# Performance work log

Measured on AMD Instinct MI355X. Metric: run time of the kernel, lower is better.

## Reference

```python
import jax, jax.numpy as jnp
import numpy as np

OBS, ACT, NTRAIN, BATCH = 8, 4, 128, 8
DIN = OBS + ACT


def setup_inputs() -> dict:
    key = jax.random.key(0)
    ks = jax.random.split(key, 11)
    f32 = jnp.float32
    m_x = jax.random.normal(ks[0], (BATCH, OBS), dtype=f32)
    A = 0.1 * jax.random.normal(ks[1], (BATCH, OBS, OBS), dtype=f32)
    s_x = A @ jnp.swapaxes(A, -1, -2) + 0.01 * jnp.eye(OBS, dtype=f32)  # SPD obs covariance
    m_u = jax.random.normal(ks[2], (BATCH, ACT), dtype=f32)
    Au = 0.1 * jax.random.normal(ks[3], (BATCH, ACT, ACT), dtype=f32)
    s_u = Au @ jnp.swapaxes(Au, -1, -2) + 0.01 * jnp.eye(ACT, dtype=f32)
    c_xu = 0.05 * jax.random.normal(ks[4], (BATCH, OBS, ACT), dtype=f32)
    X_train = jax.random.normal(ks[5], (NTRAIN, DIN), dtype=f32)
    lengthscales = jax.random.uniform(ks[6], (OBS, DIN), dtype=f32, minval=0.5, maxval=2.0)
    variances = jax.random.uniform(ks[7], (OBS, 1), dtype=f32, minval=0.5, maxval=1.5)
    noises = jax.random.uniform(ks[8], (OBS,), dtype=f32, minval=0.01, maxval=0.1)
    R = jax.random.normal(ks[9], (OBS, NTRAIN, NTRAIN), dtype=f32) / np.float32(np.sqrt(NTRAIN))
    inv_K = R @ jnp.swapaxes(R, -1, -2) + 0.1 * jnp.eye(NTRAIN, dtype=f32)  # SPD like a true K^-1
    beta = 0.1 * jax.random.normal(ks[10], (OBS, NTRAIN), dtype=f32)
    return dict(m_x=m_x, s_x=s_x, m_u=m_u, s_u=s_u, c_xu=c_xu, X_train=X_train,
                lengthscales=lengthscales, variances=variances, noises=noises,
                inv_K=inv_K, beta=beta)


def _forward(m_x, s_x, m_u, s_u, c_xu, X_train, lengthscales, variances, noises, inv_K, beta):
    obs_dim, input_dim = lengthscales.shape
    n = X_train.shape[0]
    eyeD = jnp.eye(input_dim, dtype=m_x.dtype)
    # joint input distribution over [x, u]
    joint_mean = jnp.concatenate([m_x, m_u], axis=-1)                      # [B, D]
    s_ = s_x @ c_xu                                                        # [B, obs, act] (as in source)
    upper = jnp.concatenate([s_x, s_], axis=-1)                            # [B, obs, D]
    lower = jnp.concatenate([jnp.swapaxes(s_, -1, -2), s_u], axis=-1)      # [B, act, D]
    joint_var = jnp.concatenate([upper, lower], axis=-2)                   # [B, D, D]
    # --- predictive mean (moment matching) ---
    inp = X_train[None, :, :] - joint_mean[:, None, :]                     # [B, N, D]
    inv_ls = 1.0 / lengthscales                                            # [E, D]
    inv_N = inp[:, None, :, :] * inv_ls[None, :, None, :]                  # [B, E, N, D]
    B_mat = inv_ls[None, :, :, None] * joint_var[:, None, :, :] * inv_ls[None, :, None, :] + eyeD
    t = jnp.swapaxes(jnp.linalg.solve(B_mat, jnp.swapaxes(inv_N, -1, -2)), -1, -2)  # [B, E, N, D]
    scaled_exp = jnp.exp(-0.5 * jnp.sum(inv_N * t, axis=-1))               # [B, E, N]
    lb = scaled_exp * beta[None, :, :]                                     # [B, E, N]
    det_B = jnp.linalg.det(B_mat)                                          # [B, E]
    var_v = variances[:, 0]                                                # [E]
    c = var_v[None, :] / jnp.sqrt(det_B)                                   # [B, E]
    pred_mean = jnp.sum(lb, axis=-1) * c                                   # [B, E]
    # --- input-output cross covariance ---
    t_inv_L = t * inv_ls[None, :, None, :]                                 # [B, E, N, D]
    cross_cov = jnp.swapaxes(jnp.einsum('bend,ben->bed', t_inv_L, lb) * c[..., None], -1, -2)  # [B, D, E]
    # --- predictive covariance: vectorized over all (a, b) output pairs ---
    X_i = X_train[:, None, :]
    X_j = X_train[None, :, :]
    diff = X_i - X_j                                                       # [N, N, D]
    l2 = lengthscales ** 2
    inv_l2 = 1.0 / l2

    def pair(l2_a, inv_a, var_a, beta_a, l2_b, inv_b, var_b, beta_b):
        inv_sum = inv_a + inv_b                                            # [D]
        Lam = 1.0 / inv_sum
        z_bar = Lam * (X_i * inv_a + X_j * inv_b)                          # [N, N, D]
        z = z_bar[None, :, :, :] - joint_mean[:, None, None, :]            # [B, N, N, D]
        z_flat = z.reshape(z.shape[0], n * n, input_dim)
        R_ab = joint_var * inv_sum[None, None, :] + eyeD                   # joint_var @ diag(inv_sum) + I
        exp1 = -0.5 * jnp.sum(diff * diff * (1.0 / (l2_a + l2_b)), axis=-1)  # [N, N]
        M_ab = joint_var + jnp.diag(Lam)[None, :, :]                       # [B, D, D]
        solved = jnp.swapaxes(jnp.linalg.solve(M_ab, jnp.swapaxes(z_flat, -1, -2)), -1, -2)
        exp2 = (-0.5 * jnp.sum(z_flat * solved, axis=-1)).reshape(z.shape[0], n, n)
        c_ab = var_a * var_b / jnp.sqrt(jnp.linalg.det(R_ab))              # [B]
        Q = c_ab[:, None, None] * jnp.exp(exp1[None, :, :] + exp2)         # [B, N, N]
        main = jnp.einsum('i,bij,j->b', beta_a, Q, beta_b)                 # [B]
        return main, Q

    pair_b = jax.vmap(pair, in_axes=(None, None, None, None, 0, 0, 0, 0))
    pair_ab = jax.vmap(pair_b, in_axes=(0, 0, 0, 0, None, None, None, None))
    main, Q = pair_ab(l2, inv_l2, var_v, beta, l2, inv_l2, var_v, beta)    # [E, E, B], [E, E, B, N, N]
    pred_cov = jnp.moveaxis(main, -1, 0)                                   # [B, E, E]
    idx = jnp.arange(obs_dim)
    Q_diag = Q[idx, idx]                                                   # [E, B, N, N]
    trace_val = jnp.einsum('eij,ebji->eb', inv_K, Q_diag)                  # [E, B]
    diag_corr = var_v[:, None] - trace_val + noises[:, None]               # [E, B]
    pred_cov = pred_cov + diag_corr.T[:, :, None] * jnp.eye(obs_dim, dtype=m_x.dtype)
    pred_cov = pred_cov - pred_mean[:, :, None] * pred_mean[:, None, :]
    pred_cov = 0.5 * (pred_cov + jnp.swapaxes(pred_cov, -1, -2))
    # --- propagate state moments ---
    cov_xf = upper @ cross_cov                                             # [B, obs, obs]
    m_out = m_x + pred_mean
    s_out = s_x + pred_cov + cov_xf + jnp.swapaxes(cov_xf, -1, -2)
    s_out = 0.5 * (s_out + jnp.swapaxes(s_out, -1, -2)) + 1e-8 * jnp.eye(obs_dim, dtype=m_x.dtype)
    return m_out, s_out


def reference(m_x, s_x, m_u, s_u, c_xu, X_train, lengthscales, variances, noises, inv_K, beta):
    return _forward(m_x, s_x, m_u, s_u, c_xu, X_train, lengthscales, variances, noises, inv_K, beta)
```

## Files before the change

### kernel.cpp

```cpp
#include <hip/hip_runtime.h>
#include <math.h>

#define OBS 8
#define ACT 4
#define DIN 12
#define NTRAIN 128
#define BATCH 8
#define NPAIR 36
#define NPT (BATCH*NPAIR)
#define NGT (BATCH*OBS)
#define NTASK (NPT+NGT)

#define WS_PM  0
#define WS_CC  64
#define WS_MN  832
#define WS_TR  1344

__global__ void __launch_bounds__(256) k_fused(
    const float* __restrict__ m_x, const float* __restrict__ s_x,
    const float* __restrict__ m_u, const float* __restrict__ s_u,
    const float* __restrict__ c_xu, const float* __restrict__ X,
    const float* __restrict__ ls, const float* __restrict__ vars,
    const float* __restrict__ beta, const float* __restrict__ invK,
    float* __restrict__ ws)
{
    int blk = blockIdx.x, tid = threadIdx.x;
    bool isPair = blk < NPT;
    int b, a = 0, c = 0, e = 0;
    if (isPair) {
        b = blk / NPAIR;
        int rem = blk % NPAIR;
        while (rem >= OBS - a) { rem -= OBS - a; a++; }
        c = a + rem;
    } else {
        int q = blk - NPT; b = q / OBS; e = q % OBS;
    }

    __shared__ float jvs[144];
    __shared__ float Wl[144];
    __shared__ float mu[DIN];
    __shared__ float sc_wsum[DIN], sc_iA[DIN], sc_qc[DIN], sc_lam[DIN], sc_isum[DIN];
    __shared__ float s_cab;
    __shared__ __align__(16) float h[NTRAIN][12];
    __shared__ float basei[NTRAIN], wav[NTRAIN];
    __shared__ float red[4][13];

    if (tid < 144) {
        int r = tid / 12, cl = tid % 12;
        float v;
        if (r < OBS && cl < OBS) {
            v = s_x[(b*OBS+r)*OBS + cl];
        } else if (r < OBS) {
            v = 0.f;
            #pragma unroll
            for (int k = 0; k < OBS; k++)
                v += s_x[(b*OBS+r)*OBS+k] * c_xu[(b*OBS+k)*ACT + (cl-OBS)];
        } else if (cl < OBS) {
            v = 0.f;
            #pragma unroll
            for (int k = 0; k < OBS; k++)
                v += s_x[(b*OBS+cl)*OBS+k] * c_xu[(b*OBS+k)*ACT + (r-OBS)];
        } else {
            v = s_u[(b*ACT+r-OBS)*ACT + (cl-OBS)];
        }
        jvs[tid] = v;
    } else if (tid >= 160 && tid < 172) {
        int d = tid - 160;
        mu[d] = (d < OBS) ? m_x[b*OBS+d] : m_u[b*ACT+d-OBS];
    } else if (tid >= 192 && tid < 204) {
        int d = tid - 192;
        if (isPair) {
            float la = ls[a*DIN+d]; la *= la;
            float lc = ls[c*DIN+d]; lc *= lc;
            float ia = 1.f/la, ic = 1.f/lc;
            float is = ia + ic;
            float L  = 1.f/is;
            sc_wsum[d] = 1.f/(la+lc);
            sc_iA[d] = L*ia;
            sc_qc[d] = L*ic;
            sc_lam[d] = L;
            sc_isum[d] = is;
        } else {
            sc_iA[d] = 1.f / ls[e*DIN+d];
        }
    }
    __syncthreads();

    if (tid < DIN) {
        int r = tid;
        float row[12];
        if (isPair) {
            #pragma unroll
            for (int j = 0; j < 12; j++) row[j] = jvs[r*12+j];
            row[r] += sc_lam[r];
        } else {
            float ir = sc_iA[r];
            #pragma unroll
            for (int j = 0; j < 12; j++) row[j] = ir * sc_iA[j] * jvs[r*12+j];
            row[r] += 1.f;
        }
        float det = 1.f;
        #pragma unroll
        for (int k = 0; k < 12; k++) {
            float p = __shfl(row[k], k);
            float ip = 1.f / p;
            det *= p;
            float prow[12];
            #pragma unroll
            for (int j = 0; j < 12; j++) prow[j] = __shfl(row[j], k) * ip;
            if (r == k) {
                #pragma unroll
                for (int j = 0; j < 12; j++) row[j] = prow[j];
                row[k] = ip;
            } else {
                float f = row[k];
                #pragma unroll
                for (int j = 0; j < 12; j++) if (j != k) row[j] -= f * prow[j];
                row[k] = -f * ip;
            }
        }
        #pragma unroll
        for (int j = 0; j < 12; j++) Wl[r*12+j] = row[j];
        if (r == 0) {
            if (isPair) {
                float s = det;
                #pragma unroll
                for (int d = 0; d < 12; d++) s *= sc_isum[d];
                s_cab = vars[a]*vars[c] / sqrtf(s);
            } else {
                s_cab = vars[e] / sqrtf(det);
            }
        }
    }
    __syncthreads();

    if (isPair) {
        bool diag = (a == c);
        if (tid < NTRAIN) {
            int i = tid;
            const float4* xr = (const float4*)(X + i*DIN);
            float4 x0 = xr[0], x1 = xr[1], x2 = xr[2];
            float x[12] = {x0.x,x0.y,x0.z,x0.w, x1.x,x1.y,x1.z,x1.w, x2.x,x2.y,x2.z,x2.w};
            float r[12]; float e1 = 0.f;
            #pragma unroll
            for (int d = 0; d < 12; d++) {
                r[d] = sc_iA[d]*x[d] - mu[d];
                e1 += sc_wsum[d]*x[d]*x[d];
            }
            float alpha = 0.f;
            #pragma unroll
            for (int d = 0; d < 12; d++) {
                float u = 0.f;
                #pragma unroll
                for (int cl = 0; cl < 12; cl++) u += Wl[d*12+cl]*r[cl];
                alpha += r[d]*u;
                h[i][d] = sc_wsum[d]*x[d] - u*sc_qc[d];
            }
            basei[i] = -0.5f*(e1 + alpha);
            wav[i] = beta[a*NTRAIN+i];
        }
        int j = tid & 127;
        float xj[12], basej, wc;
        {
            const float4* xr = (const float4*)(X + j*DIN);
            float4 x0 = xr[0], x1 = xr[1], x2 = xr[2];
            xj[0]=x0.x; xj[1]=x0.y; xj[2]=x0.z; xj[3]=x0.w;
            xj[4]=x1.x; xj[5]=x1.y; xj[6]=x1.z; xj[7]=x1.w;
            xj[8]=x2.x; xj[9]=x2.y; xj[10]=x2.z; xj[11]=x2.w;
            float q[12]; float e1 = 0.f;
            #pragma unroll
            for (int d = 0; d < 12; d++) {
                q[d] = sc_qc[d]*xj[d];
                e1 += sc_wsum[d]*xj[d]*xj[d];
            }
            float bq = 0.f;
            #pragma unroll
            for (int d = 0; d < 12; d++) {
                float u = 0.f;
                #pragma unroll
                for (int cl = 0; cl < 12; cl++) u += Wl[d*12+cl]*q[cl];
                bq += q[d]*u;
            }
            basej = -0.5f*(e1 + bq);
            wc = beta[c*NTRAIN+j];
        }
        __syncthreads();
        float accm = 0.f, acct = 0.f;
        const float* Ka = invK + a*NTRAIN*NTRAIN;
        int ip = tid >> 7;
        #pragma unroll 8
        for (int k = 0; k < 64; k++) {
            int i = ip + 2*k;
            const float4* hp = (const float4*)(&h[i][0]);
            float4 h0 = hp[0], h1 = hp[1], h2 = hp[2];
            float sA = fmaf(h0.x,xj[0], fmaf(h0.y,xj[1], fmaf(h0.z,xj[2], h0.w*xj[3])));
            float sB = fmaf(h1.x,xj[4], fmaf(h1.y,xj[5], fmaf(h1.z,xj[6], h1.w*xj[7])));
            float sC = fmaf(h2.x,xj[8], fmaf(h2.y,xj[9], fmaf(h2.z,xj[10], h2.w*xj[11])));
            float ev = __expf(sA + sB + sC + basei[i] + basej);
            accm = fmaf(wav[i], ev, accm);
            if (diag) acct = fmaf(Ka[i*NTRAIN+j], ev, acct);
        }
        accm *= wc;
        #pragma unroll
        for (int off = 32; off >= 1; off >>= 1) {
            accm += __shfl_xor(accm, off, 64);
            acct += __shfl_xor(acct, off, 64);
        }
        int wv = tid >> 6, lane = tid & 63;
        if (lane == 0) { red[wv][0] = accm; red[wv][1] = acct; }
        __syncthreads();
        if (tid == 0) {
            float cab = s_cab;
            float m = (red[0][0]+red[1][0]+red[2][0]+red[3][0]) * cab;
            ws[WS_MN + b*64 + a*8 + c] = m;
            ws[WS_MN + b*64 + c*8 + a] = m;
            if (diag)
                ws[WS_TR + b*8 + a] = (red[0][1]+red[1][1]+red[2][1]+red[3][1]) * cab;
        }
    } else {
        float vals[13];
        #pragma unroll
        for (int v = 0; v < 13; v++) vals[v] = 0.f;
        if (tid < NTRAIN) {
            int n = tid;
            const float4* xr = (const float4*)(X + n*DIN);
            float4 x0 = xr[0], x1 = xr[1], x2 = xr[2];
            float x[12] = {x0.x,x0.y,x0.z,x0.w, x1.x,x1.y,x1.z,x1.w, x2.x,x2.y,x2.z,x2.w};
            float iN[12];
            #pragma unroll
            for (int d = 0; d < 12; d++) iN[d] = (x[d]-mu[d]) * sc_iA[d];
            float qq = 0.f; float tv[12];
            #pragma unroll
            for (int d = 0; d < 12; d++) {
                float u = 0.f;
                #pragma unroll
                for (int cl = 0; cl < 12; cl++) u += Wl[d*12+cl]*iN[cl];
                tv[d] = u; qq += iN[d]*u;
            }
            float lb = __expf(-0.5f*qq) * beta[e*NTRAIN+n];
            vals[0] = lb;
            #pragma unroll
            for (int d = 0; d < 12; d++) vals[1+d] = tv[d]*sc_iA[d]*lb;
        }
        #pragma unroll
        for (int v = 0; v < 13; v++)
            #pragma unroll
            for (int off = 32; off >= 1; off >>= 1) vals[v] += __shfl_xor(vals[v], off, 64);
        int wv = tid >> 6, lane = tid & 63;
        if (lane == 0) {
            #pragma unroll
            for (int v = 0; v < 13; v++) red[wv][v] = vals[v];
        }
        __syncthreads();
        if (tid == 0) {
            float cn = s_cab;
            ws[WS_PM + b*OBS + e] = cn*(red[0][0]+red[1][0]+red[2][0]+red[3][0]);
            for (int d = 0; d < 12; d++)
                ws[WS_CC + (b*DIN+d)*OBS + e] =
                    cn*(red[0][1+d]+red[1][1+d]+red[2][1+d]+red[3][1+d]);
        }
    }
}

__global__ void k_final(const float* __restrict__ m_x, const float* __restrict__ s_x,
                        const float* __restrict__ c_xu, const float* __restrict__ vars,
                        const float* __restrict__ noises, const float* __restrict__ ws,
                        float* __restrict__ out) {
    int b = blockIdx.x, t = threadIdx.x;
    __shared__ float pm[OBS];
    __shared__ float sxs[64];
    const float* cc = ws + WS_CC + b*DIN*OBS;
    const float* mn = ws + WS_MN + b*64;
    const float* tr = ws + WS_TR + b*OBS;
    sxs[t] = s_x[b*64 + t];
    if (t < OBS) {
        float p = ws[WS_PM + b*OBS + t];
        pm[t] = p;
        out[b*OBS + t] = m_x[b*OBS + t] + p;
    }
    __syncthreads();
    int r = t >> 3, cl = t & 7;
    float P = mn[r*8 + cl];
    if (r == cl) P += vars[r] - tr[r] + noises[r];
    P -= pm[r]*pm[cl];
    float cxf = 0.f, cxfT = 0.f;
    #pragma unroll
    for (int d = 0; d < 8; d++) {
        cxf  += sxs[r*8+d]  * cc[d*8+cl];
        cxfT += sxs[cl*8+d] * cc[d*8+r];
    }
    #pragma unroll
    for (int d = 0; d < 4; d++) {
        float jr = 0.f, jc = 0.f;
        #pragma unroll
        for (int k = 0; k < 8; k++) {
            float cx = c_xu[(b*OBS+k)*ACT + d];
            jr += sxs[r*8+k]  * cx;
            jc += sxs[cl*8+k] * cx;
        }
        cxf  += jr * cc[(8+d)*8 + cl];
        cxfT += jc * cc[(8+d)*8 + r];
    }
    float S = sxs[r*8+cl] + P + cxf + cxfT;
    if (r == cl) S += 1e-8f;
    out[64 + b*64 + t] = S;
}

extern "C" void kernel_launch(void* const* d_in, const int* in_sizes, int n_in,
                              void* d_out, int out_size, void* d_ws, size_t ws_size,
                              hipStream_t stream) {
    const float* m_x    = (const float*)d_in[0];
    const float* s_x    = (const float*)d_in[1];
    const float* m_u    = (const float*)d_in[2];
    const float* s_u    = (const float*)d_in[3];
    const float* c_xu   = (const float*)d_in[4];
    const float* X      = (const float*)d_in[5];
    const float* ls     = (const float*)d_in[6];
    const float* vars   = (const float*)d_in[7];
    const float* noises = (const float*)d_in[8];
    const float* invK   = (const float*)d_in[9];
    const float* beta   = (const float*)d_in[10];
    float* out = (float*)d_out;
    float* ws  = (float*)d_ws;

    k_fused<<<NTASK, 256, 0, stream>>>(m_x, s_x, m_u, s_u, c_xu, X, ls, vars, beta, invK, ws);
    k_final<<<BATCH, 64, 0, stream>>>(m_x, s_x, c_xu, vars, noises, ws, out);
}
```

Measured before the change: 103.5 us.

## Fuse final kernel via last-block atomic counter and widen blocks to 512 threads

Merges the separate finalisation kernel into the main kernel: each block publishes its results with agent-scope atomic stores, increments a global counter, and the last block to finish computes the output covariance and mean. Blocks also double from 256 to 512 threads, halving the per-thread loop over training points in the pair tasks. This removes one kernel launch and its dependency gap, but adds a memset launch, fences and atomics. The non-pair branch now reduces only two wave partials, which assumes the work still fits in the first 128 threads.

```diff
diff --git a/kernel.cpp b/kernel.cpp
--- a/kernel.cpp
+++ b/kernel.cpp
@@ -10,19 +10,29 @@
 #define NPT (BATCH*NPAIR)
 #define NGT (BATCH*OBS)
 #define NTASK (NPT+NGT)
+#define THREADS 512
 
 #define WS_PM  0
 #define WS_CC  64
 #define WS_MN  832
 #define WS_TR  1344
-
-__global__ void __launch_bounds__(256) k_fused(
+#define WS_CNT 1408
+
+__device__ __forceinline__ float agload(const float* p) {
+    return __hip_atomic_load(p, __ATOMIC_RELAXED, __HIP_MEMORY_SCOPE_AGENT);
+}
+__device__ __forceinline__ void agstore(float* p, float v) {
+    __hip_atomic_store(p, v, __ATOMIC_RELAXED, __HIP_MEMORY_SCOPE_AGENT);
+}
+
+__global__ void __launch_bounds__(THREADS) k_all(
     const float* __restrict__ m_x, const float* __restrict__ s_x,
     const float* __restrict__ m_u, const float* __restrict__ s_u,
     const float* __restrict__ c_xu, const float* __restrict__ X,
     const float* __restrict__ ls, const float* __restrict__ vars,
-    const float* __restrict__ beta, const float* __restrict__ invK,
-    float* __restrict__ ws)
+    const float* __restrict__ noises, const float* __restrict__ beta,
+    const float* __restrict__ invK, float* __restrict__ ws,
+    float* __restrict__ out)
 {
     int blk = blockIdx.x, tid = threadIdx.x;
     bool isPair = blk < NPT;
@@ -43,7 +53,8 @@
     __shared__ float s_cab;
     __shared__ __align__(16) float h[NTRAIN][12];
     __shared__ float basei[NTRAIN], wav[NTRAIN];
-    __shared__ float red[4][13];
+    __shared__ float red[8][13];
+    __shared__ unsigned s_last;
 
     if (tid < 144) {
         int r = tid / 12, cl = tid % 12;
@@ -189,8 +200,8 @@
         const float* Ka = invK + a*NTRAIN*NTRAIN;
         int ip = tid >> 7;
         #pragma unroll 8
-        for (int k = 0; k < 64; k++) {
-            int i = ip + 2*k;
+        for (int k = 0; k < 32; k++) {
+            int i = ip + 4*k;
             const float4* hp = (const float4*)(&h[i][0]);
             float4 h0 = hp[0], h1 = hp[1], h2 = hp[2];
             float sA = fmaf(h0.x,xj[0], fmaf(h0.y,xj[1], fmaf(h0.z,xj[2], h0.w*xj[3])));
@@ -210,12 +221,13 @@
         if (lane == 0) { red[wv][0] = accm; red[wv][1] = acct; }
         __syncthreads();
         if (tid == 0) {
-            float cab = s_cab;
-            float m = (red[0][0]+red[1][0]+red[2][0]+red[3][0]) * cab;
-            ws[WS_MN + b*64 + a*8 + c] = m;
-            ws[WS_MN + b*64 + c*8 + a] = m;
-            if (diag)
-                ws[WS_TR + b*8 + a] = (red[0][1]+red[1][1]+red[2][1]+red[3][1]) * cab;
+            float m = 0.f, t = 0.f;
+            #pragma unroll
+            for (int w = 0; w < 8; w++) { m += red[w][0]; t += red[w][1]; }
+            m *= s_cab; t *= s_cab;
+            agstore(ws + WS_MN + b*64 + a*8 + c, m);
+            agstore(ws + WS_MN + b*64 + c*8 + a, m);
+            if (diag) agstore(ws + WS_TR + b*8 + a, t);
         }
     } else {
         float vals[13];
@@ -254,56 +266,62 @@
         __syncthreads();
         if (tid == 0) {
             float cn = s_cab;
-            ws[WS_PM + b*OBS + e] = cn*(red[0][0]+red[1][0]+red[2][0]+red[3][0]);
+            agstore(ws + WS_PM + b*OBS + e, cn*(red[0][0]+red[1][0]));
             for (int d = 0; d < 12; d++)
-                ws[WS_CC + (b*DIN+d)*OBS + e] =
-                    cn*(red[0][1+d]+red[1][1+d]+red[2][1+d]+red[3][1+d]);
-        }
-    }
-}
-
-__global__ void k_final(const float* __restrict__ m_x, const float* __restrict__ s_x,
-                        const float* __restrict__ c_xu, const float* __restrict__ vars,
-                        const float* __restrict__ noises, const float* __restrict__ ws,
-                        float* __restrict__ out) {
-    int b = blockIdx.x, t = threadIdx.x;
-    __shared__ float pm[OBS];
-    __shared__ float sxs[64];
-    const float* cc = ws + WS_CC + b*DIN*OBS;
-    const float* mn = ws + WS_MN + b*64;
-    const float* tr = ws + WS_TR + b*OBS;
-    sxs[t] = s_x[b*64 + t];
-    if (t < OBS) {
-        float p = ws[WS_PM + b*OBS + t];
-        pm[t] = p;
-        out[b*OBS + t] = m_x[b*OBS + t] + p;
+                agstore(ws + WS_CC + (b*DIN+d)*OBS + e, cn*(red[0][1+d]+red[1][1+d]));
+        }
+    }
+
+    __threadfence();
+    if (tid == 0) {
+        unsigned* cnt = (unsigned*)(ws + WS_CNT);
+        unsigned old = __hip_atomic_fetch_add(cnt, 1u, __ATOMIC_ACQ_REL,
+                                              __HIP_MEMORY_SCOPE_AGENT);
+        s_last = (old == NTASK - 1) ? 1u : 0u;
     }
     __syncthreads();
-    int r = t >> 3, cl = t & 7;
-    float P = mn[r*8 + cl];
-    if (r == cl) P += vars[r] - tr[r] + noises[r];
-    P -= pm[r]*pm[cl];
-    float cxf = 0.f, cxfT = 0.f;
-    #pragma unroll
-    for (int d = 0; d < 8; d++) {
-        cxf  += sxs[r*8+d]  * cc[d*8+cl];
-        cxfT += sxs[cl*8+d] * cc[d*8+r];
-    }
-    #pragma unroll
-    for (int d = 0; d < 4; d++) {
-        float jr = 0.f, jc = 0.f;
-        #pragma unroll
-        for (int k = 0; k < 8; k++) {
-            float cx = c_xu[(b*OBS+k)*ACT + d];
-            jr += sxs[r*8+k]  * cx;
-            jc += sxs[cl*8+k] * cx;
-        }
-        cxf  += jr * cc[(8+d)*8 + cl];
-        cxfT += jc * cc[(8+d)*8 + r];
-    }
-    float S = sxs[r*8+cl] + P + cxf + cxfT;
-    if (r == cl) S += 1e-8f;
-    out[64 + b*64 + t] = S;
+    if (s_last) {
+        __threadfence();
+        int bb = tid >> 6, t = tid & 63;
+        int r = t >> 3, cl = t & 7;
+        const float* pm = ws + WS_PM + bb*OBS;
+        const float* cc = ws + WS_CC + bb*DIN*OBS;
+        const float* mn = ws + WS_MN + bb*64;
+        const float* tr = ws + WS_TR + bb*OBS;
+        if (t < OBS)
+            out[bb*OBS + t] = m_x[bb*OBS + t] + agload(pm + t);
+        float pmr = agload(pm + r), pmc = agload(pm + cl);
+        float P = agload(mn + r*8 + cl);
+        if (r == cl) P += vars[r] - agload(tr + r) + noises[r];
+        P -= pmr * pmc;
+        float sxr[8], sxc[8];
+        #pragma unroll
+        for (int d = 0; d < 8; d++) {
+            sxr[d] = s_x[(bb*8+r)*8 + d];
+            sxc[d] = s_x[(bb*8+cl)*8 + d];
+        }
+        float cxf = 0.f, cxfT = 0.f;
+        #pragma unroll
+        for (int d = 0; d < 8; d++) {
+            cxf  += sxr[d] * agload(cc + d*8 + cl);
+            cxfT += sxc[d] * agload(cc + d*8 + r);
+        }
+        #pragma unroll
+        for (int d = 0; d < 4; d++) {
+            float jr = 0.f, jc = 0.f;
+            #pragma unroll
+            for (int k = 0; k < 8; k++) {
+                float cx = c_xu[(bb*OBS+k)*ACT + d];
+                jr += sxr[k] * cx;
+                jc += sxc[k] * cx;
+            }
+            cxf  += jr * agload(cc + (8+d)*8 + cl);
+            cxfT += jc * agload(cc + (8+d)*8 + r);
+        }
+        float S = sxr[cl] + P + cxf + cxfT;
+        if (r == cl) S += 1e-8f;
+        out[64 + bb*64 + t] = S;
+    }
 }
 
 extern "C" void kernel_launch(void* const* d_in, const int* in_sizes, int n_in,
@@ -323,6 +341,7 @@
     float* out = (float*)d_out;
     float* ws  = (float*)d_ws;
 
-    k_fused<<<NTASK, 256, 0, stream>>>(m_x, s_x, m_u, s_u, c_xu, X, ls, vars, beta, invK, ws);
-    k_final<<<BATCH, 64, 0, stream>>>(m_x, s_x, c_xu, vars, noises, ws, out);
+    hipMemsetAsync((char*)d_ws + WS_CNT*sizeof(float), 0, sizeof(unsigned), stream);
+    k_all<<<NTASK, THREADS, 0, stream>>>(m_x, s_x, m_u, s_u, c_xu, X, ls, vars,
+                                         noises, beta, invK, ws, out);
 }
```

New measurement: 134.7 us. 1.3x slower.

## Register-block two j columns per thread and pack basei/beta into padded h rows

Applied to the files above, without the earlier changes.

Each thread now handles two adjacent j columns (j0=2*lane) and the 256 threads are split as 4 waves striding over i, so each h row read from shared memory is reused for two exp evaluations. The per-row base term and beta weight are packed into a 16-float h row with a padded stride, and the diagonal invK is read as float2. X rows are loaded once at kernel start and shared between the pair and single-output paths. This aims to cut shared-memory loads and duplicated setup work per exp, at the cost of more registers. The padded h array (128x68 floats) uses much more LDS than the 16 floats per row the code reads, which may lower occupancy.

```diff
diff --git a/kernel.cpp b/kernel.cpp
--- a/kernel.cpp
+++ b/kernel.cpp
@@ -10,6 +10,7 @@
 #define NPT (BATCH*NPAIR)
 #define NGT (BATCH*OBS)
 #define NTASK (NPT+NGT)
+#define HSTRIDE 68
 
 #define WS_PM  0
 #define WS_CC  64
@@ -25,6 +26,7 @@
     float* __restrict__ ws)
 {
     int blk = blockIdx.x, tid = threadIdx.x;
+    int lane = tid & 63, w = tid >> 6;
     bool isPair = blk < NPT;
     int b, a = 0, c = 0, e = 0;
     if (isPair) {
@@ -41,9 +43,28 @@
     __shared__ float mu[DIN];
     __shared__ float sc_wsum[DIN], sc_iA[DIN], sc_qc[DIN], sc_lam[DIN], sc_isum[DIN];
     __shared__ float s_cab;
-    __shared__ __align__(16) float h[NTRAIN][12];
-    __shared__ float basei[NTRAIN], wav[NTRAIN];
+    __shared__ __align__(16) float h[NTRAIN][HSTRIDE];
     __shared__ float red[4][13];
+
+    int j0 = 2*lane;
+    float xa[12], xb[12], xi[12];
+    {
+        const float4* xr = (const float4*)(X + j0*DIN);
+        float4 t0 = xr[0], t1 = xr[1], t2 = xr[2], t3 = xr[3], t4 = xr[4], t5 = xr[5];
+        xa[0]=t0.x; xa[1]=t0.y; xa[2]=t0.z; xa[3]=t0.w;
+        xa[4]=t1.x; xa[5]=t1.y; xa[6]=t1.z; xa[7]=t1.w;
+        xa[8]=t2.x; xa[9]=t2.y; xa[10]=t2.z; xa[11]=t2.w;
+        xb[0]=t3.x; xb[1]=t3.y; xb[2]=t3.z; xb[3]=t3.w;
+        xb[4]=t4.x; xb[5]=t4.y; xb[6]=t4.z; xb[7]=t4.w;
+        xb[8]=t5.x; xb[9]=t5.y; xb[10]=t5.z; xb[11]=t5.w;
+    }
+    if (tid < NTRAIN) {
+        const float4* xr = (const float4*)(X + tid*DIN);
+        float4 t0 = xr[0], t1 = xr[1], t2 = xr[2];
+        xi[0]=t0.x; xi[1]=t0.y; xi[2]=t0.z; xi[3]=t0.w;
+        xi[4]=t1.x; xi[5]=t1.y; xi[6]=t1.z; xi[7]=t1.w;
+        xi[8]=t2.x; xi[9]=t2.y; xi[10]=t2.z; xi[11]=t2.w;
+    }
 
     if (tid < 144) {
         int r = tid / 12, cl = tid % 12;
@@ -138,15 +159,13 @@
         bool diag = (a == c);
         if (tid < NTRAIN) {
             int i = tid;
-            const float4* xr = (const float4*)(X + i*DIN);
-            float4 x0 = xr[0], x1 = xr[1], x2 = xr[2];
-            float x[12] = {x0.x,x0.y,x0.z,x0.w, x1.x,x1.y,x1.z,x1.w, x2.x,x2.y,x2.z,x2.w};
             float r[12]; float e1 = 0.f;
             #pragma unroll
             for (int d = 0; d < 12; d++) {
-                r[d] = sc_iA[d]*x[d] - mu[d];
-                e1 += sc_wsum[d]*x[d]*x[d];
-            }
+                r[d] = sc_iA[d]*xi[d] - mu[d];
+                e1 += sc_wsum[d]*xi[d]*xi[d];
+            }
+            float hrow[16];
             float alpha = 0.f;
             #pragma unroll
             for (int d = 0; d < 12; d++) {
@@ -154,68 +173,84 @@
                 #pragma unroll
                 for (int cl = 0; cl < 12; cl++) u += Wl[d*12+cl]*r[cl];
                 alpha += r[d]*u;
-                h[i][d] = sc_wsum[d]*x[d] - u*sc_qc[d];
-            }
-            basei[i] = -0.5f*(e1 + alpha);
-            wav[i] = beta[a*NTRAIN+i];
-        }
-        int j = tid & 127;
-        float xj[12], basej, wc;
+                hrow[d] = sc_wsum[d]*xi[d] - u*sc_qc[d];
+            }
+            hrow[12] = -0.5f*(e1 + alpha);
+            hrow[13] = beta[a*NTRAIN+i];
+            hrow[14] = 0.f; hrow[15] = 0.f;
+            float4* hp = (float4*)&h[i][0];
+            hp[0] = make_float4(hrow[0],hrow[1],hrow[2],hrow[3]);
+            hp[1] = make_float4(hrow[4],hrow[5],hrow[6],hrow[7]);
+            hp[2] = make_float4(hrow[8],hrow[9],hrow[10],hrow[11]);
+            hp[3] = make_float4(hrow[12],hrow[13],hrow[14],hrow[15]);
+        }
+        float basej0, basej1, wc0, wc1;
         {
-            const float4* xr = (const float4*)(X + j*DIN);
-            float4 x0 = xr[0], x1 = xr[1], x2 = xr[2];
-            xj[0]=x0.x; xj[1]=x0.y; xj[2]=x0.z; xj[3]=x0.w;
-            xj[4]=x1.x; xj[5]=x1.y; xj[6]=x1.z; xj[7]=x1.w;
-            xj[8]=x2.x; xj[9]=x2.y; xj[10]=x2.z; xj[11]=x2.w;
-            float q[12]; float e1 = 0.f;
-            #pragma unroll
-            for (int d = 0; d < 12; d++) {
-                q[d] = sc_qc[d]*xj[d];
-                e1 += sc_wsum[d]*xj[d]*xj[d];
-            }
-            float bq = 0.f;
-            #pragma unroll
-            for (int d = 0; d < 12; d++) {
-                float u = 0.f;
-                #pragma unroll
-                for (int cl = 0; cl < 12; cl++) u += Wl[d*12+cl]*q[cl];
-                bq += q[d]*u;
-            }
-            basej = -0.5f*(e1 + bq);
-            wc = beta[c*NTRAIN+j];
+            float q0[12], q1[12]; float e10 = 0.f, e11 = 0.f;
+            #pragma unroll
+            for (int d = 0; d < 12; d++) {
+                q0[d] = sc_qc[d]*xa[d];
+                q1[d] = sc_qc[d]*xb[d];
+                e10 += sc_wsum[d]*xa[d]*xa[d];
+                e11 += sc_wsum[d]*xb[d]*xb[d];
+            }
+            float bq0 = 0.f, bq1 = 0.f;
+            #pragma unroll
+            for (int d = 0; d < 12; d++) {
+                float u0 = 0.f, u1 = 0.f;
+                #pragma unroll
+                for (int cl = 0; cl < 12; cl++) {
+                    float wv = Wl[d*12+cl];
+                    u0 += wv*q0[cl];
+                    u1 += wv*q1[cl];
+                }
+                bq0 += q0[d]*u0;
+                bq1 += q1[d]*u1;
+            }
+            basej0 = -0.5f*(e10 + bq0);
+            basej1 = -0.5f*(e11 + bq1);
+            wc0 = beta[c*NTRAIN + j0];
+            wc1 = beta[c*NTRAIN + j0 + 1];
         }
         __syncthreads();
-        float accm = 0.f, acct = 0.f;
-        const float* Ka = invK + a*NTRAIN*NTRAIN;
-        int ip = tid >> 7;
-        #pragma unroll 8
-        for (int k = 0; k < 64; k++) {
-            int i = ip + 2*k;
-            const float4* hp = (const float4*)(&h[i][0]);
-            float4 h0 = hp[0], h1 = hp[1], h2 = hp[2];
-            float sA = fmaf(h0.x,xj[0], fmaf(h0.y,xj[1], fmaf(h0.z,xj[2], h0.w*xj[3])));
-            float sB = fmaf(h1.x,xj[4], fmaf(h1.y,xj[5], fmaf(h1.z,xj[6], h1.w*xj[7])));
-            float sC = fmaf(h2.x,xj[8], fmaf(h2.y,xj[9], fmaf(h2.z,xj[10], h2.w*xj[11])));
-            float ev = __expf(sA + sB + sC + basei[i] + basej);
-            accm = fmaf(wav[i], ev, accm);
-            if (diag) acct = fmaf(Ka[i*NTRAIN+j], ev, acct);
-        }
-        accm *= wc;
+        float am0 = 0.f, am1 = 0.f, at0 = 0.f, at1 = 0.f;
+        const float2* Kb = (const float2*)(invK + a*NTRAIN*NTRAIN);
+        #pragma unroll 4
+        for (int k = 0; k < 32; k++) {
+            int i = w + 4*k;
+            const float4* hp = (const float4*)&h[i][0];
+            float4 h0 = hp[0], h1 = hp[1], h2 = hp[2], h3 = hp[3];
+            float sA0 = fmaf(h0.x,xa[0], fmaf(h0.y,xa[1], fmaf(h0.z,xa[2], h0.w*xa[3])));
+            float sB0 = fmaf(h1.x,xa[4], fmaf(h1.y,xa[5], fmaf(h1.z,xa[6], h1.w*xa[7])));
+            float sC0 = fmaf(h2.x,xa[8], fmaf(h2.y,xa[9], fmaf(h2.z,xa[10], h2.w*xa[11])));
+            float sA1 = fmaf(h0.x,xb[0], fmaf(h0.y,xb[1], fmaf(h0.z,xb[2], h0.w*xb[3])));
+            float sB1 = fmaf(h1.x,xb[4], fmaf(h1.y,xb[5], fmaf(h1.z,xb[6], h1.w*xb[7])));
+            float sC1 = fmaf(h2.x,xb[8], fmaf(h2.y,xb[9], fmaf(h2.z,xb[10], h2.w*xb[11])));
+            float e0 = __expf(sA0 + sB0 + sC0 + h3.x + basej0);
+            float e1v = __expf(sA1 + sB1 + sC1 + h3.x + basej1);
+            am0 = fmaf(h3.y, e0, am0);
+            am1 = fmaf(h3.y, e1v, am1);
+            if (diag) {
+                float2 kv = Kb[i*64 + lane];
+                at0 = fmaf(kv.x, e0, at0);
+                at1 = fmaf(kv.y, e1v, at1);
+            }
+        }
+        float accm = am0*wc0 + am1*wc1;
+        float acct = at0 + at1;
         #pragma unroll
         for (int off = 32; off >= 1; off >>= 1) {
             accm += __shfl_xor(accm, off, 64);
             acct += __shfl_xor(acct, off, 64);
         }
-        int wv = tid >> 6, lane = tid & 63;
-        if (lane == 0) { red[wv][0] = accm; red[wv][1] = acct; }
+        if (lane == 0) { red[w][0] = accm; red[w][1] = acct; }
         __syncthreads();
         if (tid == 0) {
-            float cab = s_cab;
-            float m = (red[0][0]+red[1][0]+red[2][0]+red[3][0]) * cab;
+            float m = (red[0][0]+red[1][0]+red[2][0]+red[3][0]) * s_cab;
             ws[WS_MN + b*64 + a*8 + c] = m;
             ws[WS_MN + b*64 + c*8 + a] = m;
             if (diag)
-                ws[WS_TR + b*8 + a] = (red[0][1]+red[1][1]+red[2][1]+red[3][1]) * cab;
+                ws[WS_TR + b*8 + a] = (red[0][1]+red[1][1]+red[2][1]+red[3][1]) * s_cab;
         }
     } else {
         float vals[13];
@@ -223,12 +258,9 @@
         for (int v = 0; v < 13; v++) vals[v] = 0.f;
         if (tid < NTRAIN) {
             int n = tid;
-            const float4* xr = (const float4*)(X + n*DIN);
-            float4 x0 = xr[0], x1 = xr[1], x2 = xr[2];
-            float x[12] = {x0.x,x0.y,x0.z,x0.w, x1.x,x1.y,x1.z,x1.w, x2.x,x2.y,x2.z,x2.w};
             float iN[12];
             #pragma unroll
-            for (int d = 0; d < 12; d++) iN[d] = (x[d]-mu[d]) * sc_iA[d];
+            for (int d = 0; d < 12; d++) iN[d] = (xi[d]-mu[d]) * sc_iA[d];
             float qq = 0.f; float tv[12];
             #pragma unroll
             for (int d = 0; d < 12; d++) {
@@ -246,18 +278,16 @@
         for (int v = 0; v < 13; v++)
             #pragma unroll
             for (int off = 32; off >= 1; off >>= 1) vals[v] += __shfl_xor(vals[v], off, 64);
-        int wv = tid >> 6, lane = tid & 63;
         if (lane == 0) {
             #pragma unroll
-            for (int v = 0; v < 13; v++) red[wv][v] = vals[v];
+            for (int v = 0; v < 13; v++) red[w][v] = vals[v];
         }
         __syncthreads();
         if (tid == 0) {
             float cn = s_cab;
-            ws[WS_PM + b*OBS + e] = cn*(red[0][0]+red[1][0]+red[2][0]+red[3][0]);
+            ws[WS_PM + b*OBS + e] = cn*(red[0][0]+red[1][0]);
             for (int d = 0; d < 12; d++)
-                ws[WS_CC + (b*DIN+d)*OBS + e] =
-                    cn*(red[0][1+d]+red[1][1+d]+red[2][1+d]+red[3][1+d]);
+                ws[WS_CC + (b*DIN+d)*OBS + e] = cn*(red[0][1+d]+red[1][1+d]);
         }
     }
 }
@@ -323,6 +353,7 @@
     float* out = (float*)d_out;
     float* ws  = (float*)d_ws;
 
-    k_fused<<<NTASK, 256, 0, stream>>>(m_x, s_x, m_u, s_u, c_xu, X, ls, vars, beta, invK, ws);
+    k_fused<<<NTASK, 256, 0, stream>>>(m_x, s_x, m_u, s_u, c_xu, X, ls, vars,
+                                       beta, invK, ws);
     k_final<<<BATCH, 64, 0, stream>>>(m_x, s_x, c_xu, vars, noises, ws, out);
 }
```

Result: faster. 92.27 us (-10.8%).
